# Kernel tuning notes

Measured on AMD Instinct MI355X. Metric: run time of the kernel, lower is better.

Reference implementation:

```python
import jax, jax.numpy as jnp
import numpy as np

B, D, C = 4096, 1024, 11003
SCALE = 28.0
EPS_LS = 0.1
T = 4.0
L2, L3, L4 = 1.0, 1.0, 1.0
ALPHA, BETA = 0.6, 0.4
SPOS, SNEG = 10.0, 40.0
HDR_ALPHA, HDR_BETA, PLEN = 3.0, 3.0, 63


def setup_inputs() -> dict:
    key = jax.random.key(0)
    k1, k2, k3, k4, k5 = jax.random.split(key, 5)
    return {
        "visual_embed": jax.random.normal(k1, (B, D), dtype=jnp.float32),
        "textual_embed": jax.random.normal(k2, (B, D), dtype=jnp.float32),
        "labels": jax.random.randint(k3, (B,), 0, C, dtype=jnp.int64)
        if jax.config.read("jax_enable_x64") else jax.random.randint(k3, (B,), 0, C, dtype=jnp.int32),
        "W": jax.random.normal(k4, (D, C), dtype=jnp.float32) * (6.0 / (D + C)) ** 0.5,
        "W_text": jax.random.normal(k5, (D, C), dtype=jnp.float32) * (6.0 / (D + C)) ** 0.5,
    }


def _l2norm(x, axis):
    return x / jnp.linalg.norm(x, axis=axis, keepdims=True)


def _label_smooth_ce(logits, labels):
    # CrossEntropyLabelSmooth with epsilon=0.1
    lp = jax.nn.log_softmax(logits, axis=1)
    n, c = logits.shape
    picked = jnp.take_along_axis(lp, labels[:, None], axis=1)[:, 0]
    return -((1.0 - EPS_LS) * picked + (EPS_LS / c) * lp.sum(axis=1)).mean()


def _pdist(e, eps=1e-12):
    sq = (e * e).sum(axis=1)
    d2 = jnp.maximum(sq[:, None] + sq[None, :] - 2.0 * (e @ e.T), eps)
    d = jnp.sqrt(d2)
    return d * (1.0 - jnp.eye(e.shape[0], dtype=d.dtype))  # zero diagonal


def _hard_dark_rank(student, teacher):
    score_t = -HDR_ALPHA * _pdist(teacher) ** HDR_BETA
    score_s = -HDR_ALPHA * _pdist(student) ** HDR_BETA
    # top PLEN neighbors of teacher (skip self at rank 0), descending sort
    permute_idx = jnp.argsort(-score_t, axis=1)[:, 1 : PLEN + 1]  # [B, PLEN]
    ordered = jnp.take_along_axis(score_s, permute_idx, axis=1)  # [B, PLEN]
    # logsumexp over suffixes ordered[:, i:] == reversed cumulative logsumexp
    rev = jnp.flip(ordered, axis=1)
    lse_tail = jnp.flip(jax.lax.cumlogsumexp(rev, axis=1), axis=1)
    log_prob = (ordered - lse_tail).sum(axis=1)
    return (-log_prob).mean()


def _kl_div(student_logits, teacher_logits):
    s = jax.nn.softmax(student_logits / T, axis=1)
    t = jax.nn.softmax(jax.lax.stop_gradient(teacher_logits) / T, axis=1)
    log_s = jnp.log(jnp.maximum(s, 1e-12))
    log_t = jnp.log(jnp.maximum(t, 1e-12))
    return (((log_t - log_s) * t).sum(axis=1)).mean()


def reference(visual_embed, textual_embed, labels, W, W_text):
    vn = _l2norm(visual_embed, axis=1)
    tn = _l2norm(textual_embed, axis=1)
    Wn = W / jnp.linalg.norm(W, axis=0, keepdims=True)
    Wtn = W_text / jnp.linalg.norm(W_text, axis=0, keepdims=True)

    visual_logits = SCALE * (vn @ Wn)   # [B, C]
    textual_logits = SCALE * (tn @ Wn)  # [B, C]

    v_loss = _label_smooth_ce(visual_logits, labels)
    t_loss = _label_smooth_ce(textual_logits, labels)

    # distillation (LAMBDA2 feature L2 + LAMBDA3 KL on logits)
    vf = jax.lax.stop_gradient(vn)
    dist_f = ((vf - tn) ** 2).sum(axis=1).mean()
    dist_p = _kl_div(textual_logits, visual_logits)
    distillation = L2 * dist_f + L3 * dist_p

    # W_text filter CE (LAMBDA4 branch)
    t_filter = L4 * _label_smooth_ce(SCALE * (tn @ Wtn), labels)

    # HardDarkRank (Flickr30K branch): student=textual, teacher=detached visual
    loss_hdr = _hard_dark_rank(tn, jax.lax.stop_gradient(vn))

    instance = v_loss + t_loss + t_filter + distillation + 0.1 * loss_hdr

    # global_align_loss, fully vectorized. The original loops over rows AND
    # columns so every (i,j) pair is counted twice.
    sim = vn @ tn.T  # [B, B]
    mask = labels[:, None] == labels[None, :]
    loss_pos = jnp.log1p(jnp.exp(-SPOS * (sim - ALPHA)))
    loss_neg = jnp.log1p(jnp.exp(SNEG * (sim - BETA)))
    global_align = 2.0 * jnp.where(mask, loss_pos, loss_neg).sum() / sim.shape[0]

    return instance + global_align
```

## Files before the change

kernel.cpp:

```cpp
#include <hip/hip_runtime.h>
#include <math.h>

#define Bn 4096
#define Dn 1024
#define Cn 11003
#define Cpad 11008
#define NCTL 86
#define NQ 9
#define NT 32
#define NTRI 528

typedef __attribute__((ext_vector_type(8))) short bf16x8;
typedef __attribute__((ext_vector_type(4))) float f32x4;

__device__ __forceinline__ unsigned short f2bf(float f) {
  union { float f; unsigned u; } v; v.f = f;
  unsigned r = (v.u + 0x7fffu + ((v.u >> 16) & 1u)) >> 16;
  return (unsigned short)r;
}
__device__ __forceinline__ float bf2f(unsigned short h) {
  union { unsigned u; float f; } v; v.u = ((unsigned)h) << 16;
  return v.f;
}

__device__ __forceinline__ void stage16(const unsigned short* g, unsigned short* l) {
  __builtin_amdgcn_global_load_lds(
      (const __attribute__((address_space(1))) void*)g,
      (__attribute__((address_space(3))) void*)l, 16, 0, 0);
}

__device__ __forceinline__ float blk_sum256(float v, volatile float* sb) {
#pragma unroll
  for (int o = 32; o > 0; o >>= 1) v += __shfl_down(v, o, 64);
  __syncthreads();
  if ((threadIdx.x & 63) == 0) sb[threadIdx.x >> 6] = v;
  __syncthreads();
  return sb[0] + sb[1] + sb[2] + sb[3];
}

__global__ void zero_acc_k(float* acc) {
  if (threadIdx.x < 8) acc[threadIdx.x] = 0.f;
}

__global__ __launch_bounds__(256) void rownorm_k(const float* __restrict__ x,
                                                 unsigned short* __restrict__ yh,
                                                 float* __restrict__ sq) {
  __shared__ float sb[4];
  int r = blockIdx.x;
  const float* xr = x + (size_t)r * Dn;
  float s = 0.f;
  for (int k = threadIdx.x; k < Dn; k += 256) { float v = xr[k]; s += v * v; }
  s = blk_sum256(s, sb);
  float nrm = sqrtf(s);
  float s2 = 0.f;
  for (int k = threadIdx.x; k < Dn; k += 256) {
    float v = xr[k] / nrm;
    yh[(size_t)r * Dn + k] = f2bf(v);
    s2 += v * v;
  }
  s2 = blk_sum256(s2, sb);
  if (threadIdx.x == 0) sq[r] = s2;
}

__global__ __launch_bounds__(256) void colnorm_k(const float* __restrict__ W,
                                                 float* __restrict__ rn) {
  int c = blockIdx.x * 256 + threadIdx.x;
  if (c >= Cn) return;
  float s = 0.f;
  for (int d = 0; d < Dn; ++d) { float v = W[(size_t)d * Cn + c]; s += v * v; }
  rn[c] = 1.f / sqrtf(s);
}

__global__ __launch_bounds__(256) void transpose_k(const float* __restrict__ W,
                                                   const float* __restrict__ rn,
                                                   unsigned short* __restrict__ WT) {
  __shared__ float T[64][65];
  const int c0 = blockIdx.x * 64, d0 = blockIdx.y * 64;
  const int tid = threadIdx.x;
  const int cl = tid & 63;
  for (int dl = tid >> 6; dl < 64; dl += 4) {
    float v = (c0 + cl < Cn) ? W[(size_t)(d0 + dl) * Cn + c0 + cl] : 0.f;
    T[cl][dl] = v;
  }
  __syncthreads();
  const int dd = tid & 63;
  for (int co = tid >> 6; co < 64; co += 4) {
    int c = c0 + co;
    unsigned short o = 0;
    if (c < Cn) o = f2bf(T[co][dd] * rn[c]);
    WT[(size_t)c * Dn + d0 + dd] = o;
  }
}

__global__ __launch_bounds__(256, 2) void logits_vt_k(
    const unsigned short* __restrict__ vnh, const unsigned short* __restrict__ tnh,
    const unsigned short* __restrict__ WnT, float* __restrict__ part) {
  __shared__ __align__(16) unsigned short Av[128 * 64];
  __shared__ __align__(16) unsigned short At[128 * 64];
  __shared__ __align__(16) unsigned short Bs[128 * 64];
  __shared__ float qsum[7 * 128];

  const int rt = blockIdx.x, ct = blockIdx.y;
  const int r0 = rt * 128, c0 = ct * 128;
  const int tid = threadIdx.x;
  const int lane = tid & 63;
  const int wid = tid >> 6;
  const int wr = (wid >> 1) * 64, wc = (wid & 1) * 64;
  const int m = lane & 15, q = lane >> 4;

  for (int t = tid; t < 7 * 128; t += 256) qsum[t] = 0.f;

  const f32x4 zero4 = {0.f, 0.f, 0.f, 0.f};
  f32x4 accV[4][4], accT[4][4];
#pragma unroll
  for (int i = 0; i < 4; ++i)
#pragma unroll
    for (int j = 0; j < 4; ++j) { accV[i][j] = zero4; accT[i][j] = zero4; }

  const int srow = tid >> 3;
  const int skc = (tid & 7) * 8;

  for (int kk = 0; kk < 16; ++kk) {
    const int k0 = kk * 64;
#pragma unroll
    for (int p = 0; p < 4; ++p) {
      stage16(vnh + (size_t)(r0 + p * 32 + srow) * Dn + k0 + skc, Av + p * 2048 + tid * 8);
      stage16(tnh + (size_t)(r0 + p * 32 + srow) * Dn + k0 + skc, At + p * 2048 + tid * 8);
      stage16(WnT + (size_t)(c0 + p * 32 + srow) * Dn + k0 + skc, Bs + p * 2048 + tid * 8);
    }
    __syncthreads();
#pragma unroll
    for (int ks = 0; ks < 2; ++ks) {
      bf16x8 av[4], at[4], bb[4];
#pragma unroll
      for (int f = 0; f < 4; ++f) {
        av[f] = *(const bf16x8*)(Av + (wr + f * 16 + m) * 64 + ks * 32 + q * 8);
        at[f] = *(const bf16x8*)(At + (wr + f * 16 + m) * 64 + ks * 32 + q * 8);
        bb[f] = *(const bf16x8*)(Bs + (wc + f * 16 + m) * 64 + ks * 32 + q * 8);
      }
#pragma unroll
      for (int i = 0; i < 4; ++i)
#pragma unroll
        for (int j = 0; j < 4; ++j) {
          accV[i][j] = __builtin_amdgcn_mfma_f32_16x16x32_bf16(av[i], bb[j], accV[i][j], 0, 0, 0);
          accT[i][j] = __builtin_amdgcn_mfma_f32_16x16x32_bf16(at[i], bb[j], accT[i][j], 0, 0, 0);
        }
    }
    __syncthreads();
  }

#pragma unroll
  for (int i = 0; i < 4; ++i) {
#pragma unroll
    for (int r = 0; r < 4; ++r) {
      const int rowl = wr + i * 16 + q * 4 + r;
      float s0 = 0.f, s1 = 0.f, s2 = 0.f, s3 = 0.f, s6 = 0.f, s7 = 0.f, s8 = 0.f;
#pragma unroll
      for (int j = 0; j < 4; ++j) {
        int col = c0 + wc + j * 16 + m;
        if (col < Cn) {
          float V = 28.f * accV[i][j][r];
          float T = 28.f * accT[i][j][r];
          float ev4 = __expf((V - 28.f) * 0.25f);
          float et4 = __expf((T - 28.f) * 0.25f);
          float ev2 = ev4 * ev4, et2 = et4 * et4;
          s0 += ev2 * ev2;
          s1 += V;
          s2 += et2 * et2;
          s3 += T;
          s6 += ev4;
          s7 += et4;
          s8 += ev4 * (V - T);
        }
      }
#pragma unroll
      for (int o = 1; o < 16; o <<= 1) {
        s0 += __shfl_xor(s0, o, 64); s1 += __shfl_xor(s1, o, 64);
        s2 += __shfl_xor(s2, o, 64); s3 += __shfl_xor(s3, o, 64);
        s6 += __shfl_xor(s6, o, 64); s7 += __shfl_xor(s7, o, 64);
        s8 += __shfl_xor(s8, o, 64);
      }
      if (m == 0) {
        atomicAdd(&qsum[0 * 128 + rowl], s0);
        atomicAdd(&qsum[1 * 128 + rowl], s1);
        atomicAdd(&qsum[2 * 128 + rowl], s2);
        atomicAdd(&qsum[3 * 128 + rowl], s3);
        atomicAdd(&qsum[4 * 128 + rowl], s6);
        atomicAdd(&qsum[5 * 128 + rowl], s7);
        atomicAdd(&qsum[6 * 128 + rowl], s8);
      }
    }
  }
  __syncthreads();
  if (tid < 128) {
    size_t base = (size_t)ct * Bn + r0 + tid;
    const size_t qs = (size_t)NCTL * Bn;
    part[0 * qs + base] = qsum[0 * 128 + tid];
    part[1 * qs + base] = qsum[1 * 128 + tid];
    part[2 * qs + base] = qsum[2 * 128 + tid];
    part[3 * qs + base] = qsum[3 * 128 + tid];
    part[6 * qs + base] = qsum[4 * 128 + tid];
    part[7 * qs + base] = qsum[5 * 128 + tid];
    part[8 * qs + base] = qsum[6 * 128 + tid];
  }
}

__global__ __launch_bounds__(256, 2) void logits_f_k(
    const unsigned short* __restrict__ tnh, const unsigned short* __restrict__ WtnT,
    float* __restrict__ part) {
  __shared__ __align__(16) unsigned short Aa[128 * 64];
  __shared__ __align__(16) unsigned short Bs[128 * 64];
  __shared__ float qsum[2 * 128];

  const int rt = blockIdx.x, ct = blockIdx.y;
  const int r0 = rt * 128, c0 = ct * 128;
  const int tid = threadIdx.x;
  const int lane = tid & 63;
  const int wid = tid >> 6;
  const int wr = (wid >> 1) * 64, wc = (wid & 1) * 64;
  const int m = lane & 15, q = lane >> 4;

  for (int t = tid; t < 2 * 128; t += 256) qsum[t] = 0.f;

  const f32x4 zero4 = {0.f, 0.f, 0.f, 0.f};
  f32x4 acc[4][4];
#pragma unroll
  for (int i = 0; i < 4; ++i)
#pragma unroll
    for (int j = 0; j < 4; ++j) acc[i][j] = zero4;

  const int srow = tid >> 3;
  const int skc = (tid & 7) * 8;

  for (int kk = 0; kk < 16; ++kk) {
    const int k0 = kk * 64;
#pragma unroll
    for (int p = 0; p < 4; ++p) {
      stage16(tnh + (size_t)(r0 + p * 32 + srow) * Dn + k0 + skc, Aa + p * 2048 + tid * 8);
      stage16(WtnT + (size_t)(c0 + p * 32 + srow) * Dn + k0 + skc, Bs + p * 2048 + tid * 8);
    }
    __syncthreads();
#pragma unroll
    for (int ks = 0; ks < 2; ++ks) {
      bf16x8 aa[4], bb[4];
#pragma unroll
      for (int f = 0; f < 4; ++f) {
        aa[f] = *(const bf16x8*)(Aa + (wr + f * 16 + m) * 64 + ks * 32 + q * 8);
        bb[f] = *(const bf16x8*)(Bs + (wc + f * 16 + m) * 64 + ks * 32 + q * 8);
      }
#pragma unroll
      for (int i = 0; i < 4; ++i)
#pragma unroll
        for (int j = 0; j < 4; ++j)
          acc[i][j] = __builtin_amdgcn_mfma_f32_16x16x32_bf16(aa[i], bb[j], acc[i][j], 0, 0, 0);
    }
    __syncthreads();
  }

#pragma unroll
  for (int i = 0; i < 4; ++i) {
#pragma unroll
    for (int r = 0; r < 4; ++r) {
      const int rowl = wr + i * 16 + q * 4 + r;
      float s4 = 0.f, s5 = 0.f;
#pragma unroll
      for (int j = 0; j < 4; ++j) {
        int col = c0 + wc + j * 16 + m;
        if (col < Cn) {
          float F = 28.f * acc[i][j][r];
          s4 += __expf(F - 28.f);
          s5 += F;
        }
      }
#pragma unroll
      for (int o = 1; o < 16; o <<= 1) {
        s4 += __shfl_xor(s4, o, 64);
        s5 += __shfl_xor(s5, o, 64);
      }
      if (m == 0) {
        atomicAdd(&qsum[0 * 128 + rowl], s4);
        atomicAdd(&qsum[1 * 128 + rowl], s5);
      }
    }
  }
  __syncthreads();
  if (tid < 128) {
    size_t base = (size_t)ct * Bn + r0 + tid;
    const size_t qs = (size_t)NCTL * Bn;
    part[4 * qs + base] = qsum[0 * 128 + tid];
    part[5 * qs + base] = qsum[1 * 128 + tid];
  }
}

__global__ __launch_bounds__(256, 2) void gramsym_f32_k(const unsigned short* __restrict__ A,
                                                        float* __restrict__ G) {
  __shared__ __align__(16) unsigned short Aa[128 * 64];
  __shared__ __align__(16) unsigned short Bs[128 * 64];
  int t = blockIdx.x, it = 0, rem = NT;
  while (t >= rem) { t -= rem; ++it; --rem; }
  const int jt = it + t;
  const int i0 = it * 128, j0 = jt * 128;
  const int tid = threadIdx.x;
  const int lane = tid & 63;
  const int wid = tid >> 6;
  const int wr = (wid >> 1) * 64, wc = (wid & 1) * 64;
  const int m = lane & 15, q = lane >> 4;

  const f32x4 zero4 = {0.f, 0.f, 0.f, 0.f};
  f32x4 acc[4][4];
#pragma unroll
  for (int i = 0; i < 4; ++i)
#pragma unroll
    for (int j = 0; j < 4; ++j) acc[i][j] = zero4;

  const int srow = tid >> 3;
  const int skc = (tid & 7) * 8;

  for (int kk = 0; kk < 16; ++kk) {
    const int k0 = kk * 64;
#pragma unroll
    for (int p = 0; p < 4; ++p) {
      stage16(A + (size_t)(i0 + p * 32 + srow) * Dn + k0 + skc, Aa + p * 2048 + tid * 8);
      stage16(A + (size_t)(j0 + p * 32 + srow) * Dn + k0 + skc, Bs + p * 2048 + tid * 8);
    }
    __syncthreads();
#pragma unroll
    for (int ks = 0; ks < 2; ++ks) {
      bf16x8 aa[4], bb[4];
#pragma unroll
      for (int f = 0; f < 4; ++f) {
        aa[f] = *(const bf16x8*)(Aa + (wr + f * 16 + m) * 64 + ks * 32 + q * 8);
        bb[f] = *(const bf16x8*)(Bs + (wc + f * 16 + m) * 64 + ks * 32 + q * 8);
      }
#pragma unroll
      for (int i = 0; i < 4; ++i)
#pragma unroll
        for (int j = 0; j < 4; ++j)
          acc[i][j] = __builtin_amdgcn_mfma_f32_16x16x32_bf16(aa[i], bb[j], acc[i][j], 0, 0, 0);
    }
    __syncthreads();
  }
#pragma unroll
  for (int i = 0; i < 4; ++i)
#pragma unroll
    for (int j = 0; j < 4; ++j)
#pragma unroll
      for (int r = 0; r < 4; ++r) {
        int row = wr + i * 16 + q * 4 + r, col = wc + j * 16 + m;
        G[(size_t)(i0 + row) * Bn + j0 + col] = acc[i][j][r];
        if (it != jt) G[(size_t)(j0 + col) * Bn + i0 + row] = acc[i][j][r];
      }
}

__global__ __launch_bounds__(256, 2) void gramsym_bf16_k(const unsigned short* __restrict__ A,
                                                         unsigned short* __restrict__ G) {
  __shared__ __align__(16) unsigned short Aa[128 * 64];
  __shared__ __align__(16) unsigned short Bs[128 * 64];
  int t = blockIdx.x, it = 0, rem = NT;
  while (t >= rem) { t -= rem; ++it; --rem; }
  const int jt = it + t;
  const int i0 = it * 128, j0 = jt * 128;
  const int tid = threadIdx.x;
  const int lane = tid & 63;
  const int wid = tid >> 6;
  const int wr = (wid >> 1) * 64, wc = (wid & 1) * 64;
  const int m = lane & 15, q = lane >> 4;

  const f32x4 zero4 = {0.f, 0.f, 0.f, 0.f};
  f32x4 acc[4][4];
#pragma unroll
  for (int i = 0; i < 4; ++i)
#pragma unroll
    for (int j = 0; j < 4; ++j) acc[i][j] = zero4;

  const int srow = tid >> 3;
  const int skc = (tid & 7) * 8;

  for (int kk = 0; kk < 16; ++kk) {
    const int k0 = kk * 64;
#pragma unroll
    for (int p = 0; p < 4; ++p) {
      stage16(A + (size_t)(i0 + p * 32 + srow) * Dn + k0 + skc, Aa + p * 2048 + tid * 8);
      stage16(A + (size_t)(j0 + p * 32 + srow) * Dn + k0 + skc, Bs + p * 2048 + tid * 8);
    }
    __syncthreads();
#pragma unroll
    for (int ks = 0; ks < 2; ++ks) {
      bf16x8 aa[4], bb[4];
#pragma unroll
      for (int f = 0; f < 4; ++f) {
        aa[f] = *(const bf16x8*)(Aa + (wr + f * 16 + m) * 64 + ks * 32 + q * 8);
        bb[f] = *(const bf16x8*)(Bs + (wc + f * 16 + m) * 64 + ks * 32 + q * 8);
      }
#pragma unroll
      for (int i = 0; i < 4; ++i)
#pragma unroll
        for (int j = 0; j < 4; ++j)
          acc[i][j] = __builtin_amdgcn_mfma_f32_16x16x32_bf16(aa[i], bb[j], acc[i][j], 0, 0, 0);
    }
    __syncthreads();
  }
#pragma unroll
  for (int i = 0; i < 4; ++i)
#pragma unroll
    for (int j = 0; j < 4; ++j)
#pragma unroll
      for (int r = 0; r < 4; ++r) {
        int row = wr + i * 16 + q * 4 + r, col = wc + j * 16 + m;
        unsigned short h = f2bf(acc[i][j][r]);
        G[(size_t)(i0 + row) * Bn + j0 + col] = h;
        if (it != jt) G[(size_t)(j0 + col) * Bn + i0 + row] = h;
      }
}

__global__ __launch_bounds__(256, 2) void align_k(const unsigned short* __restrict__ vnh,
                                                  const unsigned short* __restrict__ tnh,
                                                  const int* __restrict__ labels,
                                                  float* __restrict__ accbuf) {
  __shared__ __align__(16) unsigned short Aa[128 * 64];
  __shared__ __align__(16) unsigned short Bs[128 * 64];
  __shared__ int li_s[128], lj_s[128];
  __shared__ float sb[4];
  const int jt = blockIdx.x, it = blockIdx.y;
  const int j0 = jt * 128, i0 = it * 128;
  const int tid = threadIdx.x;
  const int lane = tid & 63;
  const int wid = tid >> 6;
  const int wr = (wid >> 1) * 64, wc = (wid & 1) * 64;
  const int m = lane & 15, q = lane >> 4;

  if (tid < 128) li_s[tid] = labels[i0 + tid];
  else lj_s[tid - 128] = labels[j0 + tid - 128];

  const f32x4 zero4 = {0.f, 0.f, 0.f, 0.f};
  f32x4 acc[4][4];
#pragma unroll
  for (int i = 0; i < 4; ++i)
#pragma unroll
    for (int j = 0; j < 4; ++j) acc[i][j] = zero4;

  const int srow = tid >> 3;
  const int skc = (tid & 7) * 8;

  for (int kk = 0; kk < 16; ++kk) {
    const int k0 = kk * 64;
#pragma unroll
    for (int p = 0; p < 4; ++p) {
      stage16(vnh + (size_t)(i0 + p * 32 + srow) * Dn + k0 + skc, Aa + p * 2048 + tid * 8);
      stage16(tnh + (size_t)(j0 + p * 32 + srow) * Dn + k0 + skc, Bs + p * 2048 + tid * 8);
    }
    __syncthreads();
#pragma unroll
    for (int ks = 0; ks < 2; ++ks) {
      bf16x8 aa[4], bb[4];
#pragma unroll
      for (int f = 0; f < 4; ++f) {
        aa[f] = *(const bf16x8*)(Aa + (wr + f * 16 + m) * 64 + ks * 32 + q * 8);
        bb[f] = *(const bf16x8*)(Bs + (wc + f * 16 + m) * 64 + ks * 32 + q * 8);
      }
#pragma unroll
      for (int i = 0; i < 4; ++i)
#pragma unroll
        for (int j = 0; j < 4; ++j)
          acc[i][j] = __builtin_amdgcn_mfma_f32_16x16x32_bf16(aa[i], bb[j], acc[i][j], 0, 0, 0);
    }
    __syncthreads();
  }

  float ls = 0.f;
#pragma unroll
  for (int i = 0; i < 4; ++i)
#pragma unroll
    for (int r = 0; r < 4; ++r) {
      int li = li_s[wr + i * 16 + q * 4 + r];
#pragma unroll
      for (int j = 0; j < 4; ++j) {
        int lj = lj_s[wc + j * 16 + m];
        float s = acc[i][j][r];
        float x = (li == lj) ? (-10.f * (s - 0.6f)) : (40.f * (s - 0.4f));
        ls += fmaxf(x, 0.f) + __logf(1.f + __expf(-fabsf(x)));
      }
    }
  float tot = blk_sum256(ls, sb);
  if (tid == 0) atomicAdd(&accbuf[1], tot);
}

__global__ __launch_bounds__(256) void picked_k(const unsigned short* __restrict__ vnh,
                                                const unsigned short* __restrict__ tnh,
                                                const unsigned short* __restrict__ WnT,
                                                const unsigned short* __restrict__ WtnT,
                                                const int* __restrict__ labels,
                                                float* __restrict__ pv, float* __restrict__ pt,
                                                float* __restrict__ pf, float* __restrict__ df) {
  __shared__ float sb[4];
  int r = blockIdx.x;
  int lab = labels[r];
  float spv = 0.f, spt = 0.f, spf = 0.f, sdf = 0.f;
  for (int k = threadIdx.x; k < Dn; k += 256) {
    float a = bf2f(vnh[(size_t)r * Dn + k]);
    float b = bf2f(tnh[(size_t)r * Dn + k]);
    float w = bf2f(WnT[(size_t)lab * Dn + k]);
    float wt = bf2f(WtnT[(size_t)lab * Dn + k]);
    spv += a * w;
    spt += b * w;
    spf += b * wt;
    float dd = a - b;
    sdf += dd * dd;
  }
  spv = blk_sum256(spv, sb);
  spt = blk_sum256(spt, sb);
  spf = blk_sum256(spf, sb);
  sdf = blk_sum256(sdf, sb);
  if (threadIdx.x == 0) {
    pv[r] = 28.f * spv;
    pt[r] = 28.f * spt;
    pf[r] = 28.f * spf;
    df[r] = sdf;
  }
}

__global__ __launch_bounds__(256) void finalize_k(const float* __restrict__ part,
                                                  const float* __restrict__ pv,
                                                  const float* __restrict__ pt,
                                                  const float* __restrict__ pf,
                                                  const float* __restrict__ df,
                                                  float* __restrict__ accbuf) {
  __shared__ float sb[4];
  int r = blockIdx.x * 256 + threadIdx.x;
  float s[NQ];
#pragma unroll
  for (int q = 0; q < NQ; ++q) s[q] = 0.f;
  const size_t qs = (size_t)NCTL * Bn;
  for (int ct = 0; ct < NCTL; ++ct) {
#pragma unroll
    for (int q = 0; q < NQ; ++q) s[q] += part[(size_t)q * qs + (size_t)ct * Bn + r];
  }
  float lseV = logf(s[0]) + 28.f;
  float lseT = logf(s[2]) + 28.f;
  float lseF = logf(s[4]) + 28.f;
  const float invC = 1.f / (float)Cn;
  float ceV = -(0.9f * (pv[r] - lseV) + 0.1f * invC * (s[1] - (float)Cn * lseV));
  float ceT = -(0.9f * (pt[r] - lseT) + 0.1f * invC * (s[3] - (float)Cn * lseT));
  float ceF = -(0.9f * (pf[r] - lseF) + 0.1f * invC * (s[5] - (float)Cn * lseF));
  float kl = s[8] / (4.f * s[6]) + logf(s[7]) - logf(s[6]);
  float row = ceV + ceT + ceF + kl + df[r];
  float tot = blk_sum256(row, sb);
  if (threadIdx.x == 0) atomicAdd(&accbuf[0], tot / (float)Bn);
}

__device__ __forceinline__ int kswz(int j) {
  return (j & ~63) | ((j ^ (j >> 6)) & 63);
}
__device__ __forceinline__ unsigned long long shflx_u64(unsigned long long v, int o) {
  int lo = __shfl_xor((int)(unsigned)v, o, 64);
  int hi = __shfl_xor((int)(unsigned)(v >> 32), o, 64);
  return ((unsigned long long)(unsigned)hi << 32) | (unsigned)lo;
}

__global__ __launch_bounds__(256) void hdr_k(const float* __restrict__ Gv,
                                             const unsigned short* __restrict__ Gtb,
                                             const float* __restrict__ sqv,
                                             const float* __restrict__ sqt,
                                             float* __restrict__ accbuf) {
  __shared__ float key[Bn];
  __shared__ int selIdx[64];
  __shared__ float selS[64];
  const int i = blockIdx.x, tid = threadIdx.x;
  const int lane = tid & 63, wid = tid >> 6;
  const float INF = __builtin_inff();
  float sqi = sqv[i];
  const float4* gv4 = (const float4*)(Gv + (size_t)i * Bn);
  const float4* sq4 = (const float4*)sqv;
  for (int j4 = tid; j4 < Bn / 4; j4 += 256) {
    float4 g = gv4[j4];
    float4 s = sq4[j4];
    int j = j4 * 4;
    key[kswz(j + 0)] = (j + 0 == i) ? INF : fmaxf(sqi + s.x - 2.f * g.x, 1e-12f);
    key[kswz(j + 1)] = (j + 1 == i) ? INF : fmaxf(sqi + s.y - 2.f * g.y, 1e-12f);
    key[kswz(j + 2)] = (j + 2 == i) ? INF : fmaxf(sqi + s.z - 2.f * g.z, 1e-12f);
    key[kswz(j + 3)] = (j + 3 == i) ? INF : fmaxf(sqi + s.w - 2.f * g.w, 1e-12f);
  }
  __syncthreads();

  if (wid == 0) {
    unsigned long long best = ~0ull;
    for (int k = 0; k < 64; ++k) {
      int j = k * 64 + lane;
      float v = key[kswz(j)];
      unsigned long long p = ((unsigned long long)__float_as_uint(v) << 32) | (unsigned)j;
      if (p < best) best = p;
    }
    for (int it = 0; it < 63; ++it) {
      unsigned long long w = best;
#pragma unroll
      for (int o = 32; o > 0; o >>= 1) {
        unsigned long long ow = shflx_u64(w, o);
        if (ow < w) w = ow;
      }
      int bj = (int)(unsigned)w;
      if (lane == 0) selIdx[it] = bj;
      int s = bj & 63;
      int kj = (lane << 6) | s;
      int sidx = kswz(kj);
      float kv = key[sidx];
      if (kj == bj) { kv = INF; key[sidx] = INF; }
      unsigned long long p = ((unsigned long long)__float_as_uint(kv) << 32) | (unsigned)kj;
#pragma unroll
      for (int o = 32; o > 0; o >>= 1) {
        unsigned long long op = shflx_u64(p, o);
        if (op < p) p = op;
      }
      if (lane == s) best = p;
    }
  }
  __syncthreads();

  if (tid < 63) {
    int j = selIdx[tid];
    float g = bf2f(Gtb[(size_t)i * Bn + j]);
    float d2 = fmaxf(sqt[i] + sqt[j] - 2.f * g, 1e-12f);
    selS[tid] = -3.f * sqrtf(d2) * d2;
  }
  __syncthreads();

  if (tid == 0) {
    float lse = selS[62];
    float loss = 0.f;
    for (int k = 61; k >= 0; --k) {
      float a = fmaxf(lse, selS[k]);
      lse = a + logf(__expf(lse - a) + __expf(selS[k] - a));
      loss += lse - selS[k];
    }
    atomicAdd(&accbuf[2], loss);
  }
}

__global__ void combine_k(const float* __restrict__ accbuf, float* __restrict__ out) {
  out[0] = accbuf[0] + (2.f / (float)Bn) * accbuf[1] + (0.1f / (float)Bn) * accbuf[2];
}

extern "C" void kernel_launch(void* const* d_in, const int* in_sizes, int n_in,
                              void* d_out, int out_size, void* d_ws, size_t ws_size,
                              hipStream_t stream) {
  const float* ve = (const float*)d_in[0];
  const float* te = (const float*)d_in[1];
  const int* labels = (const int*)d_in[2];
  const float* W = (const float*)d_in[3];
  const float* Wt = (const float*)d_in[4];
  float* out = (float*)d_out;

  char* base = (char*)d_ws;
  size_t off = 0;
  unsigned short* vnh = (unsigned short*)(base + off);  off += (size_t)Bn * Dn * 2;
  unsigned short* tnh = (unsigned short*)(base + off);  off += (size_t)Bn * Dn * 2;
  unsigned short* WnT = (unsigned short*)(base + off);  off += (size_t)Cpad * Dn * 2;
  unsigned short* WtnT = (unsigned short*)(base + off); off += (size_t)Cpad * Dn * 2;
  float* Gv = (float*)(base + off);          off += (size_t)Bn * Bn * 4;
  unsigned short* Gtb = (unsigned short*)(base + off); off += (size_t)Bn * Bn * 2;
  float* part = (float*)(base + off);        off += (size_t)NQ * NCTL * Bn * 4;
  float* rnW = (float*)(base + off);         off += (size_t)Cpad * 4;
  float* rnWt = (float*)(base + off);        off += (size_t)Cpad * 4;
  float* sqv = (float*)(base + off);         off += (size_t)Bn * 4;
  float* sqt = (float*)(base + off);         off += (size_t)Bn * 4;
  float* pv = (float*)(base + off);          off += (size_t)Bn * 4;
  float* pt = (float*)(base + off);          off += (size_t)Bn * 4;
  float* pf = (float*)(base + off);          off += (size_t)Bn * 4;
  float* df = (float*)(base + off);          off += (size_t)Bn * 4;
  float* acc = (float*)(base + off);         off += 64;

  zero_acc_k<<<1, 64, 0, stream>>>(acc);
  rownorm_k<<<Bn, 256, 0, stream>>>(ve, vnh, sqv);
  rownorm_k<<<Bn, 256, 0, stream>>>(te, tnh, sqt);
  colnorm_k<<<(Cn + 255) / 256, 256, 0, stream>>>(W, rnW);
  colnorm_k<<<(Cn + 255) / 256, 256, 0, stream>>>(Wt, rnWt);
  transpose_k<<<dim3(Cpad / 64, Dn / 64), 256, 0, stream>>>(W, rnW, WnT);
  transpose_k<<<dim3(Cpad / 64, Dn / 64), 256, 0, stream>>>(Wt, rnWt, WtnT);
  logits_vt_k<<<dim3(Bn / 128, NCTL), 256, 0, stream>>>(vnh, tnh, WnT, part);
  logits_f_k<<<dim3(Bn / 128, NCTL), 256, 0, stream>>>(tnh, WtnT, part);
  gramsym_f32_k<<<NTRI, 256, 0, stream>>>(vnh, Gv);
  gramsym_bf16_k<<<NTRI, 256, 0, stream>>>(tnh, Gtb);
  align_k<<<dim3(Bn / 128, Bn / 128), 256, 0, stream>>>(vnh, tnh, labels, acc);
  picked_k<<<Bn, 256, 0, stream>>>(vnh, tnh, WnT, WtnT, labels, pv, pt, pf, df);
  finalize_k<<<Bn / 256, 256, 0, stream>>>(part, pv, pt, pf, df, acc);
  hdr_k<<<Bn, 256, 0, stream>>>(Gv, Gtb, sqv, sqt, acc);
  combine_k<<<1, 1, 0, stream>>>(acc, out);
}
```

Measured before the change: 1.073 ms.

## Fuse filter logits GEMM into visual/text logits kernel and swizzle LDS tiles

```diff
diff --git a/kernel.cpp b/kernel.cpp
--- a/kernel.cpp
+++ b/kernel.cpp
@@ -28,6 +28,9 @@
       (const __attribute__((address_space(1))) void*)g,
       (__attribute__((address_space(3))) void*)l, 16, 0, 0);
 }
+
+#define SRC_BLK(tid) (((tid) & 7) ^ (((tid) >> 3) & 7))
+#define FRAG(buf, R, KB) (*(const bf16x8*)((buf) + (R) * 64 + (((KB) ^ ((R) & 7)) * 8)))
 
 __device__ __forceinline__ float blk_sum256(float v, volatile float* sb) {
 #pragma unroll
@@ -92,13 +95,15 @@
   }
 }
 
-__global__ __launch_bounds__(256, 2) void logits_vt_k(
+__global__ __launch_bounds__(256, 2) void logits_k(
     const unsigned short* __restrict__ vnh, const unsigned short* __restrict__ tnh,
-    const unsigned short* __restrict__ WnT, float* __restrict__ part) {
+    const unsigned short* __restrict__ WnT, const unsigned short* __restrict__ WtnT,
+    float* __restrict__ part) {
   __shared__ __align__(16) unsigned short Av[128 * 64];
   __shared__ __align__(16) unsigned short At[128 * 64];
   __shared__ __align__(16) unsigned short Bs[128 * 64];
-  __shared__ float qsum[7 * 128];
+  __shared__ __align__(16) unsigned short Bts[128 * 64];
+  __shared__ float qsum[NQ * 128];
 
   const int rt = blockIdx.x, ct = blockIdx.y;
   const int r0 = rt * 128, c0 = ct * 128;
@@ -108,17 +113,18 @@
   const int wr = (wid >> 1) * 64, wc = (wid & 1) * 64;
   const int m = lane & 15, q = lane >> 4;
 
-  for (int t = tid; t < 7 * 128; t += 256) qsum[t] = 0.f;
+  for (int t = tid; t < NQ * 128; t += 256) qsum[t] = 0.f;
 
   const f32x4 zero4 = {0.f, 0.f, 0.f, 0.f};
-  f32x4 accV[4][4], accT[4][4];
+  f32x4 accV[4][4], accT[4][4], accF[4][4];
 #pragma unroll
   for (int i = 0; i < 4; ++i)
 #pragma unroll
-    for (int j = 0; j < 4; ++j) { accV[i][j] = zero4; accT[i][j] = zero4; }
+    for (int j = 0; j < 4; ++j) { accV[i][j] = zero4; accT[i][j] = zero4; accF[i][j] = zero4; }
 
   const int srow = tid >> 3;
-  const int skc = (tid & 7) * 8;
+  const int sblk = SRC_BLK(tid);
+  const int skc = sblk * 8;
 
   for (int kk = 0; kk < 16; ++kk) {
     const int k0 = kk * 64;
@@ -127,24 +133,29 @@
       stage16(vnh + (size_t)(r0 + p * 32 + srow) * Dn + k0 + skc, Av + p * 2048 + tid * 8);
       stage16(tnh + (size_t)(r0 + p * 32 + srow) * Dn + k0 + skc, At + p * 2048 + tid * 8);
       stage16(WnT + (size_t)(c0 + p * 32 + srow) * Dn + k0 + skc, Bs + p * 2048 + tid * 8);
+      stage16(WtnT + (size_t)(c0 + p * 32 + srow) * Dn + k0 + skc, Bts + p * 2048 + tid * 8);
     }
     __syncthreads();
 #pragma unroll
     for (int ks = 0; ks < 2; ++ks) {
-      bf16x8 av[4], at[4], bb[4];
+      const int KB = ks * 4 + q;
+      bf16x8 av[4], at[4];
 #pragma unroll
       for (int f = 0; f < 4; ++f) {
-        av[f] = *(const bf16x8*)(Av + (wr + f * 16 + m) * 64 + ks * 32 + q * 8);
-        at[f] = *(const bf16x8*)(At + (wr + f * 16 + m) * 64 + ks * 32 + q * 8);
-        bb[f] = *(const bf16x8*)(Bs + (wc + f * 16 + m) * 64 + ks * 32 + q * 8);
-      }
-#pragma unroll
-      for (int i = 0; i < 4; ++i)
-#pragma unroll
-        for (int j = 0; j < 4; ++j) {
-          accV[i][j] = __builtin_amdgcn_mfma_f32_16x16x32_bf16(av[i], bb[j], accV[i][j], 0, 0, 0);
-          accT[i][j] = __builtin_amdgcn_mfma_f32_16x16x32_bf16(at[i], bb[j], accT[i][j], 0, 0, 0);
+        av[f] = FRAG(Av, wr + f * 16 + m, KB);
+        at[f] = FRAG(At, wr + f * 16 + m, KB);
+      }
+#pragma unroll
+      for (int j = 0; j < 4; ++j) {
+        bf16x8 bb = FRAG(Bs, wc + j * 16 + m, KB);
+        bf16x8 bt = FRAG(Bts, wc + j * 16 + m, KB);
+#pragma unroll
+        for (int i = 0; i < 4; ++i) {
+          accV[i][j] = __builtin_amdgcn_mfma_f32_16x16x32_bf16(av[i], bb, accV[i][j], 0, 0, 0);
+          accT[i][j] = __builtin_amdgcn_mfma_f32_16x16x32_bf16(at[i], bb, accT[i][j], 0, 0, 0);
+          accF[i][j] = __builtin_amdgcn_mfma_f32_16x16x32_bf16(at[i], bt, accF[i][j], 0, 0, 0);
         }
+      }
     }
     __syncthreads();
   }
@@ -154,13 +165,15 @@
 #pragma unroll
     for (int r = 0; r < 4; ++r) {
       const int rowl = wr + i * 16 + q * 4 + r;
-      float s0 = 0.f, s1 = 0.f, s2 = 0.f, s3 = 0.f, s6 = 0.f, s7 = 0.f, s8 = 0.f;
+      float s0 = 0.f, s1 = 0.f, s2 = 0.f, s3 = 0.f, s4 = 0.f, s5 = 0.f,
+            s6 = 0.f, s7 = 0.f, s8 = 0.f;
 #pragma unroll
       for (int j = 0; j < 4; ++j) {
         int col = c0 + wc + j * 16 + m;
         if (col < Cn) {
           float V = 28.f * accV[i][j][r];
           float T = 28.f * accT[i][j][r];
+          float F = 28.f * accF[i][j][r];
           float ev4 = __expf((V - 28.f) * 0.25f);
           float et4 = __expf((T - 28.f) * 0.25f);
           float ev2 = ev4 * ev4, et2 = et4 * et4;
@@ -168,6 +181,8 @@
           s1 += V;
           s2 += et2 * et2;
           s3 += T;
+          s4 += __expf(F - 28.f);
+          s5 += F;
           s6 += ev4;
           s7 += et4;
           s8 += ev4 * (V - T);
@@ -177,6 +192,7 @@
       for (int o = 1; o < 16; o <<= 1) {
         s0 += __shfl_xor(s0, o, 64); s1 += __shfl_xor(s1, o, 64);
         s2 += __shfl_xor(s2, o, 64); s3 += __shfl_xor(s3, o, 64);
+        s4 += __shfl_xor(s4, o, 64); s5 += __shfl_xor(s5, o, 64);
         s6 += __shfl_xor(s6, o, 64); s7 += __shfl_xor(s7, o, 64);
         s8 += __shfl_xor(s8, o, 64);
       }
@@ -185,9 +201,11 @@
         atomicAdd(&qsum[1 * 128 + rowl], s1);
         atomicAdd(&qsum[2 * 128 + rowl], s2);
         atomicAdd(&qsum[3 * 128 + rowl], s3);
-        atomicAdd(&qsum[4 * 128 + rowl], s6);
-        atomicAdd(&qsum[5 * 128 + rowl], s7);
-        atomicAdd(&qsum[6 * 128 + rowl], s8);
+        atomicAdd(&qsum[4 * 128 + rowl], s4);
+        atomicAdd(&qsum[5 * 128 + rowl], s5);
+        atomicAdd(&qsum[6 * 128 + rowl], s6);
+        atomicAdd(&qsum[7 * 128 + rowl], s7);
+        atomicAdd(&qsum[8 * 128 + rowl], s8);
       }
     }
   }
@@ -195,104 +213,12 @@
   if (tid < 128) {
     size_t base = (size_t)ct * Bn + r0 + tid;
     const size_t qs = (size_t)NCTL * Bn;
-    part[0 * qs + base] = qsum[0 * 128 + tid];
-    part[1 * qs + base] = qsum[1 * 128 + tid];
-    part[2 * qs + base] = qsum[2 * 128 + tid];
-    part[3 * qs + base] = qsum[3 * 128 + tid];
-    part[6 * qs + base] = qsum[4 * 128 + tid];
-    part[7 * qs + base] = qsum[5 * 128 + tid];
-    part[8 * qs + base] = qsum[6 * 128 + tid];
-  }
-}
-
-__global__ __launch_bounds__(256, 2) void logits_f_k(
-    const unsigned short* __restrict__ tnh, const unsigned short* __restrict__ WtnT,
-    float* __restrict__ part) {
-  __shared__ __align__(16) unsigned short Aa[128 * 64];
-  __shared__ __align__(16) unsigned short Bs[128 * 64];
-  __shared__ float qsum[2 * 128];
-
-  const int rt = blockIdx.x, ct = blockIdx.y;
-  const int r0 = rt * 128, c0 = ct * 128;
-  const int tid = threadIdx.x;
-  const int lane = tid & 63;
-  const int wid = tid >> 6;
-  const int wr = (wid >> 1) * 64, wc = (wid & 1) * 64;
-  const int m = lane & 15, q = lane >> 4;
-
-  for (int t = tid; t < 2 * 128; t += 256) qsum[t] = 0.f;
-
-  const f32x4 zero4 = {0.f, 0.f, 0.f, 0.f};
-  f32x4 acc[4][4];
-#pragma unroll
-  for (int i = 0; i < 4; ++i)
-#pragma unroll
-    for (int j = 0; j < 4; ++j) acc[i][j] = zero4;
-
-  const int srow = tid >> 3;
-  const int skc = (tid & 7) * 8;
-
-  for (int kk = 0; kk < 16; ++kk) {
-    const int k0 = kk * 64;
-#pragma unroll
-    for (int p = 0; p < 4; ++p) {
-      stage16(tnh + (size_t)(r0 + p * 32 + srow) * Dn + k0 + skc, Aa + p * 2048 + tid * 8);
-      stage16(WtnT + (size_t)(c0 + p * 32 + srow) * Dn + k0 + skc, Bs + p * 2048 + tid * 8);
-    }
-    __syncthreads();
-#pragma unroll
-    for (int ks = 0; ks < 2; ++ks) {
-      bf16x8 aa[4], bb[4];
-#pragma unroll
-      for (int f = 0; f < 4; ++f) {
-        aa[f] = *(const bf16x8*)(Aa + (wr + f * 16 + m) * 64 + ks * 32 + q * 8);
-        bb[f] = *(const bf16x8*)(Bs + (wc + f * 16 + m) * 64 + ks * 32 + q * 8);
-      }
-#pragma unroll
-      for (int i = 0; i < 4; ++i)
-#pragma unroll
-        for (int j = 0; j < 4; ++j)
-          acc[i][j] = __builtin_amdgcn_mfma_f32_16x16x32_bf16(aa[i], bb[j], acc[i][j], 0, 0, 0);
-    }
-    __syncthreads();
-  }
-
-#pragma unroll
-  for (int i = 0; i < 4; ++i) {
-#pragma unroll
-    for (int r = 0; r < 4; ++r) {
-      const int rowl = wr + i * 16 + q * 4 + r;
-      float s4 = 0.f, s5 = 0.f;
-#pragma unroll
-      for (int j = 0; j < 4; ++j) {
-        int col = c0 + wc + j * 16 + m;
-        if (col < Cn) {
-          float F = 28.f * acc[i][j][r];
-          s4 += __expf(F - 28.f);
-          s5 += F;
-        }
-      }
-#pragma unroll
-      for (int o = 1; o < 16; o <<= 1) {
-        s4 += __shfl_xor(s4, o, 64);
-        s5 += __shfl_xor(s5, o, 64);
-      }
-      if (m == 0) {
-        atomicAdd(&qsum[0 * 128 + rowl], s4);
-        atomicAdd(&qsum[1 * 128 + rowl], s5);
-      }
-    }
-  }
-  __syncthreads();
-  if (tid < 128) {
-    size_t base = (size_t)ct * Bn + r0 + tid;
-    const size_t qs = (size_t)NCTL * Bn;
-    part[4 * qs + base] = qsum[0 * 128 + tid];
-    part[5 * qs + base] = qsum[1 * 128 + tid];
-  }
-}
-
-__global__ __launch_bounds__(256, 2) void gramsym_f32_k(const unsigned short* __restrict__ A,
+#pragma unroll
+    for (int qq = 0; qq < NQ; ++qq) part[qq * qs + base] = qsum[qq * 128 + tid];
+  }
+}
+
+__global__ __launch_bounds__(256, 3) void gramsym_f32_k(const unsigned short* __restrict__ A,
                                                         float* __restrict__ G) {
   __shared__ __align__(16) unsigned short Aa[128 * 64];
   __shared__ __align__(16) unsigned short Bs[128 * 64];
@@ -314,7 +240,7 @@
     for (int j = 0; j < 4; ++j) acc[i][j] = zero4;
 
   const int srow = tid >> 3;
-  const int skc = (tid & 7) * 8;
+  const int skc = SRC_BLK(tid) * 8;
 
   for (int kk = 0; kk < 16; ++kk) {
     const int k0 = kk * 64;
@@ -326,11 +252,12 @@
     __syncthreads();
 #pragma unroll
     for (int ks = 0; ks < 2; ++ks) {
+      const int KB = ks * 4 + q;
       bf16x8 aa[4], bb[4];
 #pragma unroll
       for (int f = 0; f < 4; ++f) {
-        aa[f] = *(const bf16x8*)(Aa + (wr + f * 16 + m) * 64 + ks * 32 + q * 8);
-        bb[f] = *(const bf16x8*)(Bs + (wc + f * 16 + m) * 64 + ks * 32 + q * 8);
+        aa[f] = FRAG(Aa, wr + f * 16 + m, KB);
+        bb[f] = FRAG(Bs, wc + f * 16 + m, KB);
       }
 #pragma unroll
       for (int i = 0; i < 4; ++i)
@@ -352,7 +279,7 @@
       }
 }
 
-__global__ __launch_bounds__(256, 2) void gramsym_bf16_k(const unsigned short* __restrict__ A,
+__global__ __launch_bounds__(256, 3) void gramsym_bf16_k(const unsigned short* __restrict__ A,
                                                          unsigned short* __restrict__ G) {
   __shared__ __align__(16) unsigned short Aa[128 * 64];
   __shared__ __align__(16) unsigned short Bs[128 * 64];
@@ -374,7 +301,7 @@
     for (int j = 0; j < 4; ++j) acc[i][j] = zero4;
 
   const int srow = tid >> 3;
-  const int skc = (tid & 7) * 8;
+  const int skc = SRC_BLK(tid) * 8;
 
   for (int kk = 0; kk < 16; ++kk) {
     const int k0 = kk * 64;
@@ -386,11 +313,12 @@
     __syncthreads();
 #pragma unroll
     for (int ks = 0; ks < 2; ++ks) {
+      const int KB = ks * 4 + q;
       bf16x8 aa[4], bb[4];
 #pragma unroll
       for (int f = 0; f < 4; ++f) {
-        aa[f] = *(const bf16x8*)(Aa + (wr + f * 16 + m) * 64 + ks * 32 + q * 8);
-        bb[f] = *(const bf16x8*)(Bs + (wc + f * 16 + m) * 64 + ks * 32 + q * 8);
+        aa[f] = FRAG(Aa, wr + f * 16 + m, KB);
+        bb[f] = FRAG(Bs, wc + f * 16 + m, KB);
       }
 #pragma unroll
       for (int i = 0; i < 4; ++i)
@@ -413,7 +341,7 @@
       }
 }
 
-__global__ __launch_bounds__(256, 2) void align_k(const unsigned short* __restrict__ vnh,
+__global__ __launch_bounds__(256, 3) void align_k(const unsigned short* __restrict__ vnh,
                                                   const unsigned short* __restrict__ tnh,
                                                   const int* __restrict__ labels,
                                                   float* __restrict__ accbuf) {
@@ -440,7 +368,7 @@
     for (int j = 0; j < 4; ++j) acc[i][j] = zero4;
 
   const int srow = tid >> 3;
-  const int skc = (tid & 7) * 8;
+  const int skc = SRC_BLK(tid) * 8;
 
   for (int kk = 0; kk < 16; ++kk) {
     const int k0 = kk * 64;
@@ -452,11 +380,12 @@
     __syncthreads();
 #pragma unroll
     for (int ks = 0; ks < 2; ++ks) {
+      const int KB = ks * 4 + q;
       bf16x8 aa[4], bb[4];
 #pragma unroll
       for (int f = 0; f < 4; ++f) {
-        aa[f] = *(const bf16x8*)(Aa + (wr + f * 16 + m) * 64 + ks * 32 + q * 8);
-        bb[f] = *(const bf16x8*)(Bs + (wc + f * 16 + m) * 64 + ks * 32 + q * 8);
+        aa[f] = FRAG(Aa, wr + f * 16 + m, KB);
+        bb[f] = FRAG(Bs, wc + f * 16 + m, KB);
       }
 #pragma unroll
       for (int i = 0; i < 4; ++i)
@@ -675,8 +604,7 @@
   colnorm_k<<<(Cn + 255) / 256, 256, 0, stream>>>(Wt, rnWt);
   transpose_k<<<dim3(Cpad / 64, Dn / 64), 256, 0, stream>>>(W, rnW, WnT);
   transpose_k<<<dim3(Cpad / 64, Dn / 64), 256, 0, stream>>>(Wt, rnWt, WtnT);
-  logits_vt_k<<<dim3(Bn / 128, NCTL), 256, 0, stream>>>(vnh, tnh, WnT, part);
-  logits_f_k<<<dim3(Bn / 128, NCTL), 256, 0, stream>>>(tnh, WtnT, part);
+  logits_k<<<dim3(Bn / 128, NCTL), 256, 0, stream>>>(vnh, tnh, WnT, WtnT, part);
   gramsym_f32_k<<<NTRI, 256, 0, stream>>>(vnh, Gv);
   gramsym_bf16_k<<<NTRI, 256, 0, stream>>>(tnh, Gtb);
   align_k<<<dim3(Bn / 128, Bn / 128), 256, 0, stream>>>(vnh, tnh, labels, acc);
```

New measurement: 1.173 ms. 1.09x slower.

## Swizzle LDS tiles to avoid bank conflicts and enlarge logits_f row tile

Applied to the files above, without the earlier changes.

```diff
diff --git a/kernel.cpp b/kernel.cpp
--- a/kernel.cpp
+++ b/kernel.cpp
@@ -28,6 +28,9 @@
       (const __attribute__((address_space(1))) void*)g,
       (__attribute__((address_space(3))) void*)l, 16, 0, 0);
 }
+
+#define SRC_BLK(tid) (((tid) & 7) ^ (((tid) >> 3) & 7))
+#define FRAG(buf, R, KB) (*(const bf16x8*)((buf) + (R) * 64 + (((KB) ^ ((R) & 7)) * 8)))
 
 __device__ __forceinline__ float blk_sum256(float v, volatile float* sb) {
 #pragma unroll
@@ -118,7 +121,7 @@
     for (int j = 0; j < 4; ++j) { accV[i][j] = zero4; accT[i][j] = zero4; }
 
   const int srow = tid >> 3;
-  const int skc = (tid & 7) * 8;
+  const int skc = SRC_BLK(tid) * 8;
 
   for (int kk = 0; kk < 16; ++kk) {
     const int k0 = kk * 64;
@@ -131,12 +134,13 @@
     __syncthreads();
 #pragma unroll
     for (int ks = 0; ks < 2; ++ks) {
+      const int KB = ks * 4 + q;
       bf16x8 av[4], at[4], bb[4];
 #pragma unroll
       for (int f = 0; f < 4; ++f) {
-        av[f] = *(const bf16x8*)(Av + (wr + f * 16 + m) * 64 + ks * 32 + q * 8);
-        at[f] = *(const bf16x8*)(At + (wr + f * 16 + m) * 64 + ks * 32 + q * 8);
-        bb[f] = *(const bf16x8*)(Bs + (wc + f * 16 + m) * 64 + ks * 32 + q * 8);
+        av[f] = FRAG(Av, wr + f * 16 + m, KB);
+        at[f] = FRAG(At, wr + f * 16 + m, KB);
+        bb[f] = FRAG(Bs, wc + f * 16 + m, KB);
       }
 #pragma unroll
       for (int i = 0; i < 4; ++i)
@@ -208,48 +212,49 @@
 __global__ __launch_bounds__(256, 2) void logits_f_k(
     const unsigned short* __restrict__ tnh, const unsigned short* __restrict__ WtnT,
     float* __restrict__ part) {
-  __shared__ __align__(16) unsigned short Aa[128 * 64];
+  __shared__ __align__(16) unsigned short Aa[256 * 64];
   __shared__ __align__(16) unsigned short Bs[128 * 64];
-  __shared__ float qsum[2 * 128];
+  __shared__ float qsum[2 * 256];
 
   const int rt = blockIdx.x, ct = blockIdx.y;
-  const int r0 = rt * 128, c0 = ct * 128;
+  const int r0 = rt * 256, c0 = ct * 128;
   const int tid = threadIdx.x;
   const int lane = tid & 63;
   const int wid = tid >> 6;
-  const int wr = (wid >> 1) * 64, wc = (wid & 1) * 64;
+  const int wr = (wid >> 1) * 128, wc = (wid & 1) * 64;
   const int m = lane & 15, q = lane >> 4;
 
-  for (int t = tid; t < 2 * 128; t += 256) qsum[t] = 0.f;
+  for (int t = tid; t < 2 * 256; t += 256) qsum[t] = 0.f;
 
   const f32x4 zero4 = {0.f, 0.f, 0.f, 0.f};
-  f32x4 acc[4][4];
-#pragma unroll
-  for (int i = 0; i < 4; ++i)
+  f32x4 acc[8][4];
+#pragma unroll
+  for (int i = 0; i < 8; ++i)
 #pragma unroll
     for (int j = 0; j < 4; ++j) acc[i][j] = zero4;
 
   const int srow = tid >> 3;
-  const int skc = (tid & 7) * 8;
+  const int skc = SRC_BLK(tid) * 8;
 
   for (int kk = 0; kk < 16; ++kk) {
     const int k0 = kk * 64;
 #pragma unroll
-    for (int p = 0; p < 4; ++p) {
+    for (int p = 0; p < 8; ++p)
       stage16(tnh + (size_t)(r0 + p * 32 + srow) * Dn + k0 + skc, Aa + p * 2048 + tid * 8);
+#pragma unroll
+    for (int p = 0; p < 4; ++p)
       stage16(WtnT + (size_t)(c0 + p * 32 + srow) * Dn + k0 + skc, Bs + p * 2048 + tid * 8);
-    }
     __syncthreads();
 #pragma unroll
     for (int ks = 0; ks < 2; ++ks) {
-      bf16x8 aa[4], bb[4];
-#pragma unroll
-      for (int f = 0; f < 4; ++f) {
-        aa[f] = *(const bf16x8*)(Aa + (wr + f * 16 + m) * 64 + ks * 32 + q * 8);
-        bb[f] = *(const bf16x8*)(Bs + (wc + f * 16 + m) * 64 + ks * 32 + q * 8);
-      }
-#pragma unroll
-      for (int i = 0; i < 4; ++i)
+      const int KB = ks * 4 + q;
+      bf16x8 aa[8], bb[4];
+#pragma unroll
+      for (int f = 0; f < 8; ++f) aa[f] = FRAG(Aa, wr + f * 16 + m, KB);
+#pragma unroll
+      for (int f = 0; f < 4; ++f) bb[f] = FRAG(Bs, wc + f * 16 + m, KB);
+#pragma unroll
+      for (int i = 0; i < 8; ++i)
 #pragma unroll
         for (int j = 0; j < 4; ++j)
           acc[i][j] = __builtin_amdgcn_mfma_f32_16x16x32_bf16(aa[i], bb[j], acc[i][j], 0, 0, 0);
@@ -258,7 +263,7 @@
   }
 
 #pragma unroll
-  for (int i = 0; i < 4; ++i) {
+  for (int i = 0; i < 8; ++i) {
 #pragma unroll
     for (int r = 0; r < 4; ++r) {
       const int rowl = wr + i * 16 + q * 4 + r;
@@ -278,21 +283,21 @@
         s5 += __shfl_xor(s5, o, 64);
       }
       if (m == 0) {
-        atomicAdd(&qsum[0 * 128 + rowl], s4);
-        atomicAdd(&qsum[1 * 128 + rowl], s5);
-      }
-    }
-  }
-  __syncthreads();
-  if (tid < 128) {
+        atomicAdd(&qsum[0 * 256 + rowl], s4);
+        atomicAdd(&qsum[1 * 256 + rowl], s5);
+      }
+    }
+  }
+  __syncthreads();
+  {
     size_t base = (size_t)ct * Bn + r0 + tid;
     const size_t qs = (size_t)NCTL * Bn;
-    part[4 * qs + base] = qsum[0 * 128 + tid];
-    part[5 * qs + base] = qsum[1 * 128 + tid];
-  }
-}
-
-__global__ __launch_bounds__(256, 2) void gramsym_f32_k(const unsigned short* __restrict__ A,
+    part[4 * qs + base] = qsum[0 * 256 + tid];
+    part[5 * qs + base] = qsum[1 * 256 + tid];
+  }
+}
+
+__global__ __launch_bounds__(256, 3) void gramsym_f32_k(const unsigned short* __restrict__ A,
                                                         float* __restrict__ G) {
   __shared__ __align__(16) unsigned short Aa[128 * 64];
   __shared__ __align__(16) unsigned short Bs[128 * 64];
@@ -314,7 +319,7 @@
     for (int j = 0; j < 4; ++j) acc[i][j] = zero4;
 
   const int srow = tid >> 3;
-  const int skc = (tid & 7) * 8;
+  const int skc = SRC_BLK(tid) * 8;
 
   for (int kk = 0; kk < 16; ++kk) {
     const int k0 = kk * 64;
@@ -326,11 +331,12 @@
     __syncthreads();
 #pragma unroll
     for (int ks = 0; ks < 2; ++ks) {
+      const int KB = ks * 4 + q;
       bf16x8 aa[4], bb[4];
 #pragma unroll
       for (int f = 0; f < 4; ++f) {
-        aa[f] = *(const bf16x8*)(Aa + (wr + f * 16 + m) * 64 + ks * 32 + q * 8);
-        bb[f] = *(const bf16x8*)(Bs + (wc + f * 16 + m) * 64 + ks * 32 + q * 8);
+        aa[f] = FRAG(Aa, wr + f * 16 + m, KB);
+        bb[f] = FRAG(Bs, wc + f * 16 + m, KB);
       }
 #pragma unroll
       for (int i = 0; i < 4; ++i)
@@ -352,7 +358,7 @@
       }
 }
 
-__global__ __launch_bounds__(256, 2) void gramsym_bf16_k(const unsigned short* __restrict__ A,
+__global__ __launch_bounds__(256, 3) void gramsym_bf16_k(const unsigned short* __restrict__ A,
                                                          unsigned short* __restrict__ G) {
   __shared__ __align__(16) unsigned short Aa[128 * 64];
   __shared__ __align__(16) unsigned short Bs[128 * 64];
@@ -374,7 +380,7 @@
     for (int j = 0; j < 4; ++j) acc[i][j] = zero4;
 
   const int srow = tid >> 3;
-  const int skc = (tid & 7) * 8;
+  const int skc = SRC_BLK(tid) * 8;
 
   for (int kk = 0; kk < 16; ++kk) {
     const int k0 = kk * 64;
@@ -386,11 +392,12 @@
     __syncthreads();
 #pragma unroll
     for (int ks = 0; ks < 2; ++ks) {
+      const int KB = ks * 4 + q;
       bf16x8 aa[4], bb[4];
 #pragma unroll
       for (int f = 0; f < 4; ++f) {
-        aa[f] = *(const bf16x8*)(Aa + (wr + f * 16 + m) * 64 + ks * 32 + q * 8);
-        bb[f] = *(const bf16x8*)(Bs + (wc + f * 16 + m) * 64 + ks * 32 + q * 8);
+        aa[f] = FRAG(Aa, wr + f * 16 + m, KB);
+        bb[f] = FRAG(Bs, wc + f * 16 + m, KB);
       }
 #pragma unroll
       for (int i = 0; i < 4; ++i)
@@ -413,7 +420,7 @@
       }
 }
 
-__global__ __launch_bounds__(256, 2) void align_k(const unsigned short* __restrict__ vnh,
+__global__ __launch_bounds__(256, 3) void align_k(const unsigned short* __restrict__ vnh,
                                                   const unsigned short* __restrict__ tnh,
                                                   const int* __restrict__ labels,
                                                   float* __restrict__ accbuf) {
@@ -440,7 +447,7 @@
     for (int j = 0; j < 4; ++j) acc[i][j] = zero4;
 
   const int srow = tid >> 3;
-  const int skc = (tid & 7) * 8;
+  const int skc = SRC_BLK(tid) * 8;
 
   for (int kk = 0; kk < 16; ++kk) {
     const int k0 = kk * 64;
@@ -452,11 +459,12 @@
     __syncthreads();
 #pragma unroll
     for (int ks = 0; ks < 2; ++ks) {
+      const int KB = ks * 4 + q;
       bf16x8 aa[4], bb[4];
 #pragma unroll
       for (int f = 0; f < 4; ++f) {
-        aa[f] = *(const bf16x8*)(Aa + (wr + f * 16 + m) * 64 + ks * 32 + q * 8);
-        bb[f] = *(const bf16x8*)(Bs + (wc + f * 16 + m) * 64 + ks * 32 + q * 8);
+        aa[f] = FRAG(Aa, wr + f * 16 + m, KB);
+        bb[f] = FRAG(Bs, wc + f * 16 + m, KB);
       }
 #pragma unroll
       for (int i = 0; i < 4; ++i)
@@ -676,7 +684,7 @@
   transpose_k<<<dim3(Cpad / 64, Dn / 64), 256, 0, stream>>>(W, rnW, WnT);
   transpose_k<<<dim3(Cpad / 64, Dn / 64), 256, 0, stream>>>(Wt, rnWt, WtnT);
   logits_vt_k<<<dim3(Bn / 128, NCTL), 256, 0, stream>>>(vnh, tnh, WnT, part);
-  logits_f_k<<<dim3(Bn / 128, NCTL), 256, 0, stream>>>(tnh, WtnT, part);
+  logits_f_k<<<dim3(Bn / 256, NCTL), 256, 0, stream>>>(tnh, WtnT, part);
   gramsym_f32_k<<<NTRI, 256, 0, stream>>>(vnh, Gv);
   gramsym_bf16_k<<<NTRI, 256, 0, stream>>>(tnh, Gtb);
   align_k<<<dim3(Bn / 128, Bn / 128), 256, 0, stream>>>(vnh, tnh, labels, acc);
```

After: 979.0 us. -8.7%, faster.
